# Performance work log

Hardware: AMD Instinct MI355X
Metric: run time of the kernel (lower is better)

Reference implementation:

```python
import jax, jax.numpy as jnp
import numpy as np

H = 8          # num_heads in nn.MultiheadAttention
TOP_K = 3
LN_EPS = 1e-5


def _layer_norm(x, gamma, beta):
    mu = x.mean(axis=-1, keepdims=True)
    var = ((x - mu) ** 2).mean(axis=-1, keepdims=True)
    return (x - mu) * jax.lax.rsqrt(var + LN_EPS) * gamma + beta


def setup_inputs() -> dict:
    key = jax.random.key(0)
    ks = jax.random.split(key, 12)
    B, T, D, N = 4, 4096, 1024, 64
    s = 0.02
    return {
        "current_frame": jax.random.normal(ks[0], (B, T, D), jnp.float32),
        "entity_memory": jax.random.normal(ks[1], (B, N, D), jnp.float32),
        "in_proj_w": jax.random.normal(ks[2], (3 * D, D), jnp.float32) * s,
        "in_proj_b": jax.random.normal(ks[3], (3 * D,), jnp.float32) * s,
        "out_proj_w": jax.random.normal(ks[4], (D, D), jnp.float32) * s,
        "out_proj_b": jax.random.normal(ks[5], (D,), jnp.float32) * s,
        "ln_gamma": jnp.ones((3, D), jnp.float32),
        "ln_beta": jnp.zeros((3, D), jnp.float32),
        "w1": jax.random.normal(ks[6], (3, 2 * D, D), jnp.float32) * s,
        "b1": jax.random.normal(ks[7], (3, 2 * D), jnp.float32) * s,
        "w2": jax.random.normal(ks[8], (3, D, 2 * D), jnp.float32) * s,
        "b2": jax.random.normal(ks[9], (3, D), jnp.float32) * s,
        "gate_w": jax.random.normal(ks[10], (D, 2 * D), jnp.float32) * s,
        "gate_b": jax.random.normal(ks[11], (D,), jnp.float32) * s,
    }


def reference(current_frame, entity_memory, in_proj_w, in_proj_b,
              out_proj_w, out_proj_b, ln_gamma, ln_beta, w1, b1, w2, b2,
              gate_w, gate_b):
    B, T, D = current_frame.shape
    N = entity_memory.shape[1]
    hd = D // H

    # --- nn.MultiheadAttention(q=frame, k=v=entity_memory), batch_first ---
    wq, wk, wv = in_proj_w[:D], in_proj_w[D:2 * D], in_proj_w[2 * D:]
    bq, bk, bv = in_proj_b[:D], in_proj_b[D:2 * D], in_proj_b[2 * D:]
    q = (current_frame @ wq.T + bq).reshape(B, T, H, hd).transpose(0, 2, 1, 3)
    k = (entity_memory @ wk.T + bk).reshape(B, N, H, hd).transpose(0, 2, 1, 3)
    v = (entity_memory @ wv.T + bv).reshape(B, N, H, hd).transpose(0, 2, 1, 3)
    scores = jnp.einsum('bhtd,bhnd->bhtn', q, k) / jnp.sqrt(jnp.float32(hd))
    attn = jax.nn.softmax(scores, axis=-1)                     # [B,H,T,N]
    ctx = jnp.einsum('bhtn,bhnd->bhtd', attn, v)
    ctx = ctx.transpose(0, 2, 1, 3).reshape(B, T, D)
    attended = ctx @ out_proj_w.T + out_proj_b
    attn_weights = attn.mean(axis=1)                           # avg over heads [B,T,N]

    # --- residual consistency MLP stack ---
    x = current_frame + attended
    for i in range(ln_gamma.shape[0]):
        h = _layer_norm(x, ln_gamma[i], ln_beta[i])
        h = jax.nn.gelu(h @ w1[i].T + b1[i], approximate=False)
        x = x + h @ w2[i].T + b2[i]

    # --- gated EMA entity-memory update ---
    frame_summary = current_frame.mean(axis=1, keepdims=True)   # [B,1,D]
    mem_summary = entity_memory.mean(axis=1, keepdims=True)     # [B,1,D]
    gate = jax.nn.sigmoid(
        jnp.concatenate([frame_summary, mem_summary], axis=-1) @ gate_w.T + gate_b)
    new_mem = gate * frame_summary + (1.0 - gate) * mem_summary  # [B,1,D]

    top_k = min(TOP_K, N)
    topk_idx = jax.lax.top_k(attn_weights.mean(axis=1), top_k)[1]  # [B,k]
    bidx = jnp.arange(B)[:, None]
    old = entity_memory[bidx, topk_idx]                          # [B,k,D]
    entity_memory = entity_memory.at[bidx, topk_idx].set(0.7 * old + 0.3 * new_mem)

    return x, entity_memory
```

## Files before the change

### kernel.cpp

```cpp
#include <hip/hip_runtime.h>
#include <hip/hip_bf16.h>
#include <cmath>

#define B_  4
#define T_  4096
#define D_  1024
#define N_  64
#define H_  8
#define HD_ 128
#define BT_ (B_*T_)
#define D2_ 2048

typedef __attribute__((ext_vector_type(8))) short bfrag8;
typedef __attribute__((ext_vector_type(4))) float f32x4;

__device__ __forceinline__ void gload_lds16(const void* g, void* l) {
    __builtin_amdgcn_global_load_lds(
        (const __attribute__((address_space(1))) unsigned int*)g,
        (__attribute__((address_space(3))) unsigned int*)l,
        16, 0, 0);
}

template<bool GELU, bool RES, bool OUTBF16>
__global__ __launch_bounds__(256) void gemm_bf16_kernel(
    const __hip_bfloat16* __restrict__ A, const __hip_bfloat16* __restrict__ Wt,
    const float* __restrict__ bias, const float* __restrict__ res,
    void* __restrict__ Cout, int M, int N, int K)
{
    __shared__ short As[128 * 32];
    __shared__ short Bs[128 * 32];

    const int tid = threadIdx.x;
    const int lane = tid & 63;
    const int wid = tid >> 6;
    const int wr = wid >> 1, wc = wid & 1;

    const int nwg = gridDim.x * gridDim.y;
    int lin = blockIdx.y * gridDim.x + blockIdx.x;
    lin = (lin & 7) * (nwg >> 3) + (lin >> 3);
    const int by = lin / gridDim.x;
    const int bx = lin - by * gridDim.x;
    const int m0 = by * 128;
    const int n0 = bx * 128;

    const int srow = tid >> 2;
    const int scol = (tid & 3) * 8;
    const short* Ag = (const short*)A;
    const short* Bg = (const short*)Wt;

    const int frow = lane & 15;
    const int fk   = (lane >> 4) * 8;

    f32x4 acc[4][4] = {};

    for (int k0 = 0; k0 < K; k0 += 32) {
        __syncthreads();
        gload_lds16(Ag + (size_t)(m0 + srow) * K + k0 + scol,       &As[tid * 8]);
        gload_lds16(Ag + (size_t)(m0 + 64 + srow) * K + k0 + scol,  &As[2048 + tid * 8]);
        gload_lds16(Bg + (size_t)(n0 + srow) * K + k0 + scol,       &Bs[tid * 8]);
        gload_lds16(Bg + (size_t)(n0 + 64 + srow) * K + k0 + scol,  &Bs[2048 + tid * 8]);
        __syncthreads();

        bfrag8 a[4], b[4];
#pragma unroll
        for (int i = 0; i < 4; ++i)
            a[i] = *(const bfrag8*)&As[(wr * 64 + i * 16 + frow) * 32 + fk];
#pragma unroll
        for (int j = 0; j < 4; ++j)
            b[j] = *(const bfrag8*)&Bs[(wc * 64 + j * 16 + frow) * 32 + fk];
#pragma unroll
        for (int i = 0; i < 4; ++i)
#pragma unroll
            for (int j = 0; j < 4; ++j)
                acc[i][j] = __builtin_amdgcn_mfma_f32_16x16x32_bf16(a[i], b[j], acc[i][j], 0, 0, 0);
    }

#pragma unroll
    for (int i = 0; i < 4; ++i) {
        const int rbase = m0 + wr * 64 + i * 16 + (lane >> 4) * 4;
#pragma unroll
        for (int r = 0; r < 4; ++r) {
            const size_t rowoff = (size_t)(rbase + r) * N;
#pragma unroll
            for (int j = 0; j < 4; ++j) {
                const int col = n0 + wc * 64 + j * 16 + (lane & 15);
                float v = acc[i][j][r] + bias[col];
                if (GELU) v = 0.5f * v * (1.0f + erff(v * 0.70710678118654752f));
                if (RES)  v += res[rowoff + col];
                if (OUTBF16) ((__hip_bfloat16*)Cout)[rowoff + col] = __float2bfloat16(v);
                else         ((float*)Cout)[rowoff + col] = v;
            }
        }
    }
}

__global__ __launch_bounds__(256) void cvt_kernel(
    const float* __restrict__ in, __hip_bfloat16* __restrict__ out, int n)
{
    const int i = (blockIdx.x * 256 + threadIdx.x) * 8;
    if (i >= n) return;
    const float4 v0 = *(const float4*)&in[i];
    const float4 v1 = *(const float4*)&in[i + 4];
    __hip_bfloat16 o[8];
    o[0] = __float2bfloat16(v0.x); o[1] = __float2bfloat16(v0.y);
    o[2] = __float2bfloat16(v0.z); o[3] = __float2bfloat16(v0.w);
    o[4] = __float2bfloat16(v1.x); o[5] = __float2bfloat16(v1.y);
    o[6] = __float2bfloat16(v1.z); o[7] = __float2bfloat16(v1.w);
    *(uint4*)&out[i] = *(uint4*)o;
}

__global__ __launch_bounds__(256) void ln_fused_kernel(
    const float* __restrict__ x, const float* __restrict__ g,
    const float* __restrict__ be, __hip_bfloat16* __restrict__ out)
{
    const int m = blockIdx.x;
    const int c = threadIdx.x * 4;
    const float4 v = *(const float4*)&x[(size_t)m * D_ + c];
    float s = v.x + v.y + v.z + v.w;
    float ss = v.x * v.x + v.y * v.y + v.z * v.z + v.w * v.w;
#pragma unroll
    for (int off = 32; off; off >>= 1) {
        s += __shfl_xor(s, off);
        ss += __shfl_xor(ss, off);
    }
    __shared__ float bs[4], bss[4];
    const int wave = threadIdx.x >> 6;
    if ((threadIdx.x & 63) == 0) { bs[wave] = s; bss[wave] = ss; }
    __syncthreads();
    const float S = bs[0] + bs[1] + bs[2] + bs[3];
    const float SS = bss[0] + bss[1] + bss[2] + bss[3];
    const float mean = S * (1.0f / D_);
    const float rstd = rsqrtf(SS * (1.0f / D_) - mean * mean + 1e-5f);
    const float4 gg = *(const float4*)&g[c];
    const float4 bb = *(const float4*)&be[c];
    __hip_bfloat16 o[4];
    o[0] = __float2bfloat16((v.x - mean) * rstd * gg.x + bb.x);
    o[1] = __float2bfloat16((v.y - mean) * rstd * gg.y + bb.y);
    o[2] = __float2bfloat16((v.z - mean) * rstd * gg.z + bb.z);
    o[3] = __float2bfloat16((v.w - mean) * rstd * gg.w + bb.w);
    *(uint2*)&out[(size_t)m * D_ + c] = *(uint2*)o;
}

__global__ __launch_bounds__(256) void vtrans_kernel(
    const __hip_bfloat16* __restrict__ vbb, __hip_bfloat16* __restrict__ vtb)
{
    const int bh = blockIdx.x;
    const int b = bh >> 3, h = bh & 7;
    for (int ii = threadIdx.x; ii < HD_ * N_; ii += 256) {
        const int d = ii >> 6, n = ii & 63;
        vtb[(size_t)bh * (HD_ * N_) + ii] =
            vbb[(size_t)(b * N_ + n) * D_ + h * HD_ + d];
    }
}

__global__ __launch_bounds__(256) void attn_mfma_kernel(
    const __hip_bfloat16* __restrict__ qb, const __hip_bfloat16* __restrict__ kbb,
    const __hip_bfloat16* __restrict__ vtb, __hip_bfloat16* __restrict__ ctxb,
    float* __restrict__ S)
{
    const int bh = blockIdx.y;
    const int b = bh >> 3, hh = bh & 7;
    const int t0 = blockIdx.x * 128;

    __shared__ short Ql[128 * 128];
    __shared__ short Kl[64 * 128];
    __shared__ short Vtl[128 * 64];
    __shared__ __hip_bfloat16 Pl[128 * 64];

    const int tid = threadIdx.x;
    const int lane = tid & 63;
    const int wid = tid >> 6;

    const short* qg = (const short*)qb;
    for (int s = wid; s < 32; s += 4) {
        const int row = 4 * s + (lane >> 4);
        const int col8 = (lane & 15) ^ (row & 7);
        gload_lds16(qg + ((size_t)(b * T_ + t0 + row)) * D_ + hh * HD_ + col8 * 8,
                    &Ql[s * 512 + lane * 8]);
    }
    const short* kg = (const short*)kbb;
    for (int s = wid; s < 16; s += 4) {
        const int row = 4 * s + (lane >> 4);
        const int col8 = (lane & 15) ^ (row & 7);
        gload_lds16(kg + ((size_t)(b * N_ + row)) * D_ + hh * HD_ + col8 * 8,
                    &Kl[s * 512 + lane * 8]);
    }
    const short* vg = (const short*)vtb + (size_t)bh * (HD_ * N_);
    for (int s = wid; s < 16; s += 4) {
        const int row = 8 * s + (lane >> 3);
        const int col8 = (lane & 7) ^ (row & 7);
        gload_lds16(vg + row * 64 + col8 * 8, &Vtl[s * 512 + lane * 8]);
    }
    __syncthreads();

    const int frow = lane & 15;
    const int fk8  = lane >> 4;

    f32x4 acc[2][4] = {};
#pragma unroll
    for (int ks = 0; ks < 4; ++ks) {
        bfrag8 a[2], bf[4];
#pragma unroll
        for (int i = 0; i < 2; ++i) {
            const int row = wid * 32 + i * 16 + frow;
            const int col8 = (ks * 4 + fk8) ^ (row & 7);
            a[i] = *(const bfrag8*)&Ql[row * 128 + col8 * 8];
        }
#pragma unroll
        for (int j = 0; j < 4; ++j) {
            const int row = j * 16 + frow;
            const int col8 = (ks * 4 + fk8) ^ (row & 7);
            bf[j] = *(const bfrag8*)&Kl[row * 128 + col8 * 8];
        }
#pragma unroll
        for (int i = 0; i < 2; ++i)
#pragma unroll
            for (int j = 0; j < 4; ++j)
                acc[i][j] = __builtin_amdgcn_mfma_f32_16x16x32_bf16(a[i], bf[j], acc[i][j], 0, 0, 0);
    }

    const float scale = 0.088388347648318441f;
    float accS[4] = {0.f, 0.f, 0.f, 0.f};
#pragma unroll
    for (int i = 0; i < 2; ++i) {
#pragma unroll
        for (int r = 0; r < 4; ++r) {
            float sv[4];
            float m = -INFINITY;
#pragma unroll
            for (int j = 0; j < 4; ++j) { sv[j] = acc[i][j][r] * scale; m = fmaxf(m, sv[j]); }
#pragma unroll
            for (int off = 1; off < 16; off <<= 1) m = fmaxf(m, __shfl_xor(m, off));
            float sum = 0.f;
#pragma unroll
            for (int j = 0; j < 4; ++j) { sv[j] = __expf(sv[j] - m); sum += sv[j]; }
#pragma unroll
            for (int off = 1; off < 16; off <<= 1) sum += __shfl_xor(sum, off);
            const float inv = 1.0f / sum;
            const int row = wid * 32 + i * 16 + (lane >> 4) * 4 + r;
#pragma unroll
            for (int j = 0; j < 4; ++j) {
                const float pn = sv[j] * inv;
                accS[j] += pn;
                const int col = j * 16 + (lane & 15);
                Pl[row * 64 + (((col >> 3) ^ (row & 7)) << 3) + (col & 7)] = __float2bfloat16(pn);
            }
        }
    }
#pragma unroll
    for (int j = 0; j < 4; ++j) {
        float v = accS[j];
        v += __shfl_xor(v, 16);
        v += __shfl_xor(v, 32);
        if (lane < 16)
            atomicAdd(&S[b * N_ + j * 16 + lane], v * (1.0f / (H_ * (float)T_)));
    }
    __syncthreads();

    f32x4 acc2[2][8] = {};
#pragma unroll
    for (int ks = 0; ks < 2; ++ks) {
        bfrag8 pa[2];
#pragma unroll
        for (int i = 0; i < 2; ++i) {
            const int row = wid * 32 + i * 16 + frow;
            const int col8 = (ks * 4 + fk8) ^ (row & 7);
            pa[i] = *(const bfrag8*)&Pl[row * 64 + col8 * 8];
        }
#pragma unroll
        for (int j = 0; j < 8; ++j) {
            const int row = j * 16 + frow;
            const int col8 = (ks * 4 + fk8) ^ (row & 7);
            const bfrag8 vv = *(const bfrag8*)&Vtl[row * 64 + col8 * 8];
#pragma unroll
            for (int i = 0; i < 2; ++i)
                acc2[i][j] = __builtin_amdgcn_mfma_f32_16x16x32_bf16(pa[i], vv, acc2[i][j], 0, 0, 0);
        }
    }

    short* Cl = Ql;
#pragma unroll
    for (int i = 0; i < 2; ++i)
#pragma unroll
        for (int r = 0; r < 4; ++r) {
            const int row = wid * 32 + i * 16 + (lane >> 4) * 4 + r;
#pragma unroll
            for (int j = 0; j < 8; ++j) {
                __hip_bfloat16 hv = __float2bfloat16(acc2[i][j][r]);
                Cl[row * 128 + j * 16 + (lane & 15)] = *(short*)&hv;
            }
        }
    __syncthreads();
    short* cg = (short*)ctxb;
#pragma unroll
    for (int s = 0; s < 8; ++s) {
        const int c = s * 256 + tid;
        const int row = c >> 4;
        const int slot = c & 15;
        *(uint4*)&cg[((size_t)(b * T_ + t0 + row)) * D_ + hh * HD_ + slot * 8] =
            *(const uint4*)&Cl[row * 128 + slot * 8];
    }
}

__global__ __launch_bounds__(256) void frame_summary_kernel(
    const float* __restrict__ cf, float* __restrict__ fs)
{
    const int b = blockIdx.x;
    const int d = blockIdx.y * 256 + threadIdx.x;
    const int t0 = blockIdx.z * 512;
    float s = 0.0f;
    for (int t = t0; t < t0 + 512; ++t)
        s += cf[((size_t)(b * T_ + t)) * D_ + d];
    atomicAdd(&fs[b * D_ + d], s * (1.0f / (float)T_));
}

__global__ __launch_bounds__(256) void mem_summary_kernel(
    const float* __restrict__ em, float* __restrict__ ms)
{
    const int b = blockIdx.x;
    const int d = blockIdx.y * 256 + threadIdx.x;
    float s = 0.0f;
#pragma unroll 4
    for (int n = 0; n < N_; ++n)
        s += em[((size_t)(b * N_ + n)) * D_ + d];
    ms[b * D_ + d] = s * (1.0f / (float)N_);
}

__global__ __launch_bounds__(256) void gate_kernel(
    const float* __restrict__ fs, const float* __restrict__ ms,
    const float* __restrict__ gw, const float* __restrict__ gb,
    float* __restrict__ nm)
{
    const int b = blockIdx.x;
    const int d = blockIdx.y * 256 + threadIdx.x;
    const float* wrow = gw + (size_t)d * D2_;
    const float* f = fs + b * D_;
    const float* mm = ms + b * D_;
    float g = gb[d];
    for (int j = 0; j < D_; ++j) g += f[j] * wrow[j];
    for (int j = 0; j < D_; ++j) g += mm[j] * wrow[D_ + j];
    const float sig = 1.0f / (1.0f + __expf(-g));
    nm[b * D_ + d] = sig * f[d] + (1.0f - sig) * mm[d];
}

__global__ __launch_bounds__(256) void topk_update_kernel(
    const float* __restrict__ S, const float* __restrict__ em,
    const float* __restrict__ nm, float* __restrict__ emo)
{
    const int b = blockIdx.x;
    __shared__ int topi[3];
    const int tid = threadIdx.x;
    if (tid < 64) {
        float sv = S[b * N_ + tid];
#pragma unroll
        for (int k = 0; k < 3; ++k) {
            float v = sv;
            int idx = tid;
#pragma unroll
            for (int off = 32; off; off >>= 1) {
                const float ov = __shfl_xor(v, off);
                const int oi = __shfl_xor(idx, off);
                if (ov > v || (ov == v && oi < idx)) { v = ov; idx = oi; }
            }
            if (tid == 0) topi[k] = idx;
            if (tid == idx) sv = -INFINITY;
        }
    }
    __syncthreads();
    const int i0 = topi[0], i1 = topi[1], i2 = topi[2];
    const float4* emb = (const float4*)(em + (size_t)b * N_ * D_);
    const float4* nmb = (const float4*)(nm + (size_t)b * D_);
    float4* outb = (float4*)(emo + (size_t)b * N_ * D_);
    for (int idx = tid; idx < N_ * D_ / 4; idx += 256) {
        const int n = idx >> 8;
        const int d4 = idx & 255;
        float4 v = emb[idx];
        if (n == i0 || n == i1 || n == i2) {
            const float4 nv = nmb[d4];
            v.x = 0.7f * v.x + 0.3f * nv.x;
            v.y = 0.7f * v.y + 0.3f * nv.y;
            v.z = 0.7f * v.z + 0.3f * nv.z;
            v.w = 0.7f * v.w + 0.3f * nv.w;
        }
        outb[idx] = v;
    }
}

extern "C" void kernel_launch(void* const* d_in, const int* in_sizes, int n_in,
                              void* d_out, int out_size, void* d_ws, size_t ws_size,
                              hipStream_t stream)
{
    const float* cf  = (const float*)d_in[0];
    const float* em  = (const float*)d_in[1];
    const float* ipw = (const float*)d_in[2];
    const float* ipb = (const float*)d_in[3];
    const float* opw = (const float*)d_in[4];
    const float* opb = (const float*)d_in[5];
    const float* lng = (const float*)d_in[6];
    const float* lnb = (const float*)d_in[7];
    const float* w1  = (const float*)d_in[8];
    const float* b1  = (const float*)d_in[9];
    const float* w2  = (const float*)d_in[10];
    const float* b2  = (const float*)d_in[11];
    const float* gw  = (const float*)d_in[12];
    const float* gb  = (const float*)d_in[13];

    float* x   = (float*)d_out;
    float* emo = x + (size_t)BT_ * D_;

    char* w = (char*)d_ws;
    __hip_bfloat16* h    = (__hip_bfloat16*)w;
    __hip_bfloat16* qbuf = (__hip_bfloat16*)w;
    w += 67108864;
    __hip_bfloat16* actb = (__hip_bfloat16*)w; w += 33554432;
    __hip_bfloat16* ipwb = (__hip_bfloat16*)w; w += 6291456;
    __hip_bfloat16* opwb = (__hip_bfloat16*)w; w += 2097152;
    __hip_bfloat16* w1b  = (__hip_bfloat16*)w; w += 12582912;
    __hip_bfloat16* w2b  = (__hip_bfloat16*)w; w += 12582912;
    __hip_bfloat16* emb  = (__hip_bfloat16*)w; w += 524288;
    __hip_bfloat16* kbb  = (__hip_bfloat16*)w; w += 524288;
    __hip_bfloat16* vbb  = (__hip_bfloat16*)w; w += 524288;
    __hip_bfloat16* vtb  = (__hip_bfloat16*)w; w += 524288;
    float* S  = (float*)w; w += 1024;
    float* fs = (float*)w; w += 16384;
    float* ms = (float*)w; w += 16384;
    float* nm = (float*)w; w += 16384;

    hipMemsetAsync(S, 0, (256 + 4096) * sizeof(float), stream);

    const dim3 blk(256);

    cvt_kernel<<<8192, blk, 0, stream>>>(cf, actb, BT_ * D_);
    cvt_kernel<<<128,  blk, 0, stream>>>(em, emb, B_ * N_ * D_);
    cvt_kernel<<<1536, blk, 0, stream>>>(ipw, ipwb, 3 * D_ * D_);
    cvt_kernel<<<512,  blk, 0, stream>>>(opw, opwb, D_ * D_);
    cvt_kernel<<<3072, blk, 0, stream>>>(w1, w1b, 3 * D2_ * D_);
    cvt_kernel<<<3072, blk, 0, stream>>>(w2, w2b, 3 * D_ * D2_);

    gemm_bf16_kernel<false, false, true><<<dim3(8, 128), blk, 0, stream>>>(
        actb, ipwb, ipb, nullptr, qbuf, BT_, D_, D_);
    gemm_bf16_kernel<false, false, true><<<dim3(8, 2), blk, 0, stream>>>(
        emb, ipwb + D_ * D_, ipb + D_, nullptr, kbb, B_ * N_, D_, D_);
    gemm_bf16_kernel<false, false, true><<<dim3(8, 2), blk, 0, stream>>>(
        emb, ipwb + 2 * D_ * D_, ipb + 2 * D_, nullptr, vbb, B_ * N_, D_, D_);
    vtrans_kernel<<<B_ * H_, blk, 0, stream>>>(vbb, vtb);

    attn_mfma_kernel<<<dim3(T_ / 128, B_ * H_), blk, 0, stream>>>(
        qbuf, kbb, vtb, actb, S);

    gemm_bf16_kernel<false, true, false><<<dim3(8, 128), blk, 0, stream>>>(
        actb, opwb, opb, cf, x, BT_, D_, D_);

    for (int i = 0; i < 3; ++i) {
        ln_fused_kernel<<<BT_, blk, 0, stream>>>(
            x, lng + i * D_, lnb + i * D_, actb);
        gemm_bf16_kernel<true, false, true><<<dim3(16, 128), blk, 0, stream>>>(
            actb, w1b + (size_t)i * D2_ * D_, b1 + i * D2_, nullptr, h,
            BT_, D2_, D_);
        gemm_bf16_kernel<false, true, false><<<dim3(8, 128), blk, 0, stream>>>(
            h, w2b + (size_t)i * D_ * D2_, b2 + i * D_, x, x,
            BT_, D_, D2_);
    }

    frame_summary_kernel<<<dim3(B_, 4, 8), blk, 0, stream>>>(cf, fs);
    mem_summary_kernel<<<dim3(B_, 4), blk, 0, stream>>>(em, ms);
    gate_kernel<<<dim3(B_, 4), blk, 0, stream>>>(fs, ms, gw, gb, nm);
    topk_update_kernel<<<B_, blk, 0, stream>>>(S, em, nm, emo);
}
```

Baseline: 1.282 ms.

## Enlarge GEMM tiles to 256x256 with double-buffered swizzled LDS staging

The bf16 GEMM moves from 128x128 tiles with K-step 32 and 256 threads to 256x256 tiles with K-step 64 and 512 threads. The global-to-LDS loads are double-buffered so the next K tile is fetched while MFMAs run on the current one, and an XOR swizzle on the LDS column offset is meant to avoid bank conflicts. Bias loads are hoisted out of the epilogue loop. Each thread now holds 128 accumulator floats and each block uses 128KB of LDS, so occupancy drops to one block per CU. The launch bound asks for two blocks per CU, which may force register spills.

```diff
diff --git a/kernel.cpp b/kernel.cpp
--- a/kernel.cpp
+++ b/kernel.cpp
@@ -22,69 +22,96 @@
 }
 
 template<bool GELU, bool RES, bool OUTBF16>
-__global__ __launch_bounds__(256) void gemm_bf16_kernel(
+__global__ __launch_bounds__(512, 2) void gemm_bf16_kernel(
     const __hip_bfloat16* __restrict__ A, const __hip_bfloat16* __restrict__ Wt,
     const float* __restrict__ bias, const float* __restrict__ res,
     void* __restrict__ Cout, int M, int N, int K)
 {
-    __shared__ short As[128 * 32];
-    __shared__ short Bs[128 * 32];
+    __shared__ short As[2 * 256 * 64];
+    __shared__ short Bs[2 * 256 * 64];
 
     const int tid = threadIdx.x;
     const int lane = tid & 63;
     const int wid = tid >> 6;
-    const int wr = wid >> 1, wc = wid & 1;
+    const int wr = wid >> 2;
+    const int wc = wid & 3;
 
     const int nwg = gridDim.x * gridDim.y;
     int lin = blockIdx.y * gridDim.x + blockIdx.x;
-    lin = (lin & 7) * (nwg >> 3) + (lin >> 3);
+    if ((nwg & 7) == 0) lin = (lin & 7) * (nwg >> 3) + (lin >> 3);
     const int by = lin / gridDim.x;
     const int bx = lin - by * gridDim.x;
-    const int m0 = by * 128;
-    const int n0 = bx * 128;
-
-    const int srow = tid >> 2;
-    const int scol = (tid & 3) * 8;
+    const int m0 = by * 256;
+    const int n0 = bx * 256;
+
     const short* Ag = (const short*)A;
     const short* Bg = (const short*)Wt;
 
     const int frow = lane & 15;
-    const int fk   = (lane >> 4) * 8;
-
-    f32x4 acc[4][4] = {};
-
-    for (int k0 = 0; k0 < K; k0 += 32) {
+    const int fk8  = lane >> 4;
+
+    f32x4 acc[8][4] = {};
+
+    const int nt = K >> 6;
+
+    auto STAGE = [&](int t) {
+        const int kb = t << 6;
+        short* Ab = &As[(t & 1) * 16384];
+        short* Bb = &Bs[(t & 1) * 16384];
+#pragma unroll
+        for (int s = 0; s < 4; ++s) {
+            const int L = s * 512 + tid;
+            const int row = L >> 3, p = L & 7;
+            const int g8 = ((p ^ (row & 7)) << 3);
+            gload_lds16(Ag + (size_t)(m0 + row) * K + kb + g8, &Ab[L * 8]);
+            gload_lds16(Bg + (size_t)(n0 + row) * K + kb + g8, &Bb[L * 8]);
+        }
+    };
+
+    STAGE(0);
+    asm volatile("s_waitcnt vmcnt(0)" ::: "memory");
+    __syncthreads();
+
+    for (int t = 0; t < nt; ++t) {
+        if (t + 1 < nt) STAGE(t + 1);
+        const short* Ab = &As[(t & 1) * 16384];
+        const short* Bb = &Bs[(t & 1) * 16384];
+        for (int kk = 0; kk < 2; ++kk) {
+            bfrag8 a[8], b[4];
+#pragma unroll
+            for (int i = 0; i < 8; ++i) {
+                const int row = wr * 128 + i * 16 + frow;
+                a[i] = *(const bfrag8*)&Ab[row * 64 + (((kk * 4 + fk8) ^ (row & 7)) << 3)];
+            }
+#pragma unroll
+            for (int j = 0; j < 4; ++j) {
+                const int row = wc * 64 + j * 16 + frow;
+                b[j] = *(const bfrag8*)&Bb[row * 64 + (((kk * 4 + fk8) ^ (row & 7)) << 3)];
+            }
+#pragma unroll
+            for (int i = 0; i < 8; ++i)
+#pragma unroll
+                for (int j = 0; j < 4; ++j)
+                    acc[i][j] = __builtin_amdgcn_mfma_f32_16x16x32_bf16(a[i], b[j], acc[i][j], 0, 0, 0);
+        }
+        asm volatile("s_waitcnt vmcnt(0)" ::: "memory");
         __syncthreads();
-        gload_lds16(Ag + (size_t)(m0 + srow) * K + k0 + scol,       &As[tid * 8]);
-        gload_lds16(Ag + (size_t)(m0 + 64 + srow) * K + k0 + scol,  &As[2048 + tid * 8]);
-        gload_lds16(Bg + (size_t)(n0 + srow) * K + k0 + scol,       &Bs[tid * 8]);
-        gload_lds16(Bg + (size_t)(n0 + 64 + srow) * K + k0 + scol,  &Bs[2048 + tid * 8]);
-        __syncthreads();
-
-        bfrag8 a[4], b[4];
-#pragma unroll
-        for (int i = 0; i < 4; ++i)
-            a[i] = *(const bfrag8*)&As[(wr * 64 + i * 16 + frow) * 32 + fk];
-#pragma unroll
-        for (int j = 0; j < 4; ++j)
-            b[j] = *(const bfrag8*)&Bs[(wc * 64 + j * 16 + frow) * 32 + fk];
-#pragma unroll
-        for (int i = 0; i < 4; ++i)
-#pragma unroll
-            for (int j = 0; j < 4; ++j)
-                acc[i][j] = __builtin_amdgcn_mfma_f32_16x16x32_bf16(a[i], b[j], acc[i][j], 0, 0, 0);
-    }
-
-#pragma unroll
-    for (int i = 0; i < 4; ++i) {
-        const int rbase = m0 + wr * 64 + i * 16 + (lane >> 4) * 4;
+    }
+
+    float bias4[4];
+#pragma unroll
+    for (int j = 0; j < 4; ++j)
+        bias4[j] = bias[n0 + wc * 64 + j * 16 + (lane & 15)];
+#pragma unroll
+    for (int i = 0; i < 8; ++i) {
+        const int rbase = m0 + wr * 128 + i * 16 + (lane >> 4) * 4;
 #pragma unroll
         for (int r = 0; r < 4; ++r) {
             const size_t rowoff = (size_t)(rbase + r) * N;
 #pragma unroll
             for (int j = 0; j < 4; ++j) {
                 const int col = n0 + wc * 64 + j * 16 + (lane & 15);
-                float v = acc[i][j][r] + bias[col];
+                float v = acc[i][j][r] + bias4[j];
                 if (GELU) v = 0.5f * v * (1.0f + erff(v * 0.70710678118654752f));
                 if (RES)  v += res[rowoff + col];
                 if (OUTBF16) ((__hip_bfloat16*)Cout)[rowoff + col] = __float2bfloat16(v);
@@ -429,6 +456,7 @@
     hipMemsetAsync(S, 0, (256 + 4096) * sizeof(float), stream);
 
     const dim3 blk(256);
+    const dim3 blk512(512);
 
     cvt_kernel<<<8192, blk, 0, stream>>>(cf, actb, BT_ * D_);
     cvt_kernel<<<128,  blk, 0, stream>>>(em, emb, B_ * N_ * D_);
@@ -437,27 +465,27 @@
     cvt_kernel<<<3072, blk, 0, stream>>>(w1, w1b, 3 * D2_ * D_);
     cvt_kernel<<<3072, blk, 0, stream>>>(w2, w2b, 3 * D_ * D2_);
 
-    gemm_bf16_kernel<false, false, true><<<dim3(8, 128), blk, 0, stream>>>(
+    gemm_bf16_kernel<false, false, true><<<dim3(4, 64), blk512, 0, stream>>>(
         actb, ipwb, ipb, nullptr, qbuf, BT_, D_, D_);
-    gemm_bf16_kernel<false, false, true><<<dim3(8, 2), blk, 0, stream>>>(
+    gemm_bf16_kernel<false, false, true><<<dim3(4, 1), blk512, 0, stream>>>(
         emb, ipwb + D_ * D_, ipb + D_, nullptr, kbb, B_ * N_, D_, D_);
-    gemm_bf16_kernel<false, false, true><<<dim3(8, 2), blk, 0, stream>>>(
+    gemm_bf16_kernel<false, false, true><<<dim3(4, 1), blk512, 0, stream>>>(
         emb, ipwb + 2 * D_ * D_, ipb + 2 * D_, nullptr, vbb, B_ * N_, D_, D_);
     vtrans_kernel<<<B_ * H_, blk, 0, stream>>>(vbb, vtb);
 
     attn_mfma_kernel<<<dim3(T_ / 128, B_ * H_), blk, 0, stream>>>(
         qbuf, kbb, vtb, actb, S);
 
-    gemm_bf16_kernel<false, true, false><<<dim3(8, 128), blk, 0, stream>>>(
+    gemm_bf16_kernel<false, true, false><<<dim3(4, 64), blk512, 0, stream>>>(
         actb, opwb, opb, cf, x, BT_, D_, D_);
 
     for (int i = 0; i < 3; ++i) {
         ln_fused_kernel<<<BT_, blk, 0, stream>>>(
             x, lng + i * D_, lnb + i * D_, actb);
-        gemm_bf16_kernel<true, false, true><<<dim3(16, 128), blk, 0, stream>>>(
+        gemm_bf16_kernel<true, false, true><<<dim3(8, 64), blk512, 0, stream>>>(
             actb, w1b + (size_t)i * D2_ * D_, b1 + i * D2_, nullptr, h,
             BT_, D2_, D_);
-        gemm_bf16_kernel<false, true, false><<<dim3(8, 128), blk, 0, stream>>>(
+        gemm_bf16_kernel<false, true, false><<<dim3(4, 64), blk512, 0, stream>>>(
             h, w2b + (size_t)i * D_ * D2_, b2 + i * D_, x, x,
             BT_, D_, D2_);
     }
```

Measured after the change: 1.166 ms. -9.0%, faster.

## Double GEMM K-tile to 64 with XOR-swizzled LDS and fuse K/V projections

Applied to the files above, without the earlier changes.

The bf16 GEMM now stages 64-wide K slices per iteration instead of 32, using an XOR swizzle on the LDS layout to avoid bank conflicts. This halves the number of barrier pairs per K loop and gives two MFMA sub-steps per load phase. The K and V projection GEMMs are merged into one launch writing a combined KV buffer, and the attention and transpose kernels index into it. The grid remap is now guarded for grid sizes that are not multiples of 8. LDS use per block doubles, which may reduce occupancy.

```diff
diff --git a/kernel.cpp b/kernel.cpp
--- a/kernel.cpp
+++ b/kernel.cpp
@@ -27,8 +27,8 @@
     const float* __restrict__ bias, const float* __restrict__ res,
     void* __restrict__ Cout, int M, int N, int K)
 {
-    __shared__ short As[128 * 32];
-    __shared__ short Bs[128 * 32];
+    __shared__ short As[128 * 64];
+    __shared__ short Bs[128 * 64];
 
     const int tid = threadIdx.x;
     const int lane = tid & 63;
@@ -37,42 +37,55 @@
 
     const int nwg = gridDim.x * gridDim.y;
     int lin = blockIdx.y * gridDim.x + blockIdx.x;
-    lin = (lin & 7) * (nwg >> 3) + (lin >> 3);
+    if ((nwg & 7) == 0) lin = (lin & 7) * (nwg >> 3) + (lin >> 3);
     const int by = lin / gridDim.x;
     const int bx = lin - by * gridDim.x;
     const int m0 = by * 128;
     const int n0 = bx * 128;
 
-    const int srow = tid >> 2;
-    const int scol = (tid & 3) * 8;
-    const short* Ag = (const short*)A;
-    const short* Bg = (const short*)Wt;
+    const short* Ag = (const short*)A + (size_t)m0 * K;
+    const short* Bg = (const short*)Wt + (size_t)n0 * K;
 
     const int frow = lane & 15;
-    const int fk   = (lane >> 4) * 8;
+    const int fk8  = lane >> 4;
 
     f32x4 acc[4][4] = {};
 
-    for (int k0 = 0; k0 < K; k0 += 32) {
+    for (int kb = 0; kb < K; kb += 64) {
         __syncthreads();
-        gload_lds16(Ag + (size_t)(m0 + srow) * K + k0 + scol,       &As[tid * 8]);
-        gload_lds16(Ag + (size_t)(m0 + 64 + srow) * K + k0 + scol,  &As[2048 + tid * 8]);
-        gload_lds16(Bg + (size_t)(n0 + srow) * K + k0 + scol,       &Bs[tid * 8]);
-        gload_lds16(Bg + (size_t)(n0 + 64 + srow) * K + k0 + scol,  &Bs[2048 + tid * 8]);
+#pragma unroll
+        for (int s = 0; s < 4; ++s) {
+            const int L = s * 256 + tid;
+            const int row = L >> 3, p = L & 7;
+            gload_lds16(Ag + (size_t)row * K + kb + ((p ^ (row & 7)) << 3), &As[L * 8]);
+        }
+#pragma unroll
+        for (int s = 0; s < 4; ++s) {
+            const int L = s * 256 + tid;
+            const int row = L >> 3, p = L & 7;
+            gload_lds16(Bg + (size_t)row * K + kb + ((p ^ (row & 7)) << 3), &Bs[L * 8]);
+        }
         __syncthreads();
 
-        bfrag8 a[4], b[4];
-#pragma unroll
-        for (int i = 0; i < 4; ++i)
-            a[i] = *(const bfrag8*)&As[(wr * 64 + i * 16 + frow) * 32 + fk];
-#pragma unroll
-        for (int j = 0; j < 4; ++j)
-            b[j] = *(const bfrag8*)&Bs[(wc * 64 + j * 16 + frow) * 32 + fk];
-#pragma unroll
-        for (int i = 0; i < 4; ++i)
-#pragma unroll
-            for (int j = 0; j < 4; ++j)
-                acc[i][j] = __builtin_amdgcn_mfma_f32_16x16x32_bf16(a[i], b[j], acc[i][j], 0, 0, 0);
+#pragma unroll
+        for (int kk = 0; kk < 2; ++kk) {
+            bfrag8 a[4], b[4];
+#pragma unroll
+            for (int i = 0; i < 4; ++i) {
+                const int row = wr * 64 + i * 16 + frow;
+                a[i] = *(const bfrag8*)&As[row * 64 + (((kk * 4 + fk8) ^ (row & 7)) << 3)];
+            }
+#pragma unroll
+            for (int j = 0; j < 4; ++j) {
+                const int row = wc * 64 + j * 16 + frow;
+                b[j] = *(const bfrag8*)&Bs[row * 64 + (((kk * 4 + fk8) ^ (row & 7)) << 3)];
+            }
+#pragma unroll
+            for (int i = 0; i < 4; ++i)
+#pragma unroll
+                for (int j = 0; j < 4; ++j)
+                    acc[i][j] = __builtin_amdgcn_mfma_f32_16x16x32_bf16(a[i], b[j], acc[i][j], 0, 0, 0);
+        }
     }
 
 #pragma unroll
@@ -142,19 +155,19 @@
 }
 
 __global__ __launch_bounds__(256) void vtrans_kernel(
-    const __hip_bfloat16* __restrict__ vbb, __hip_bfloat16* __restrict__ vtb)
+    const __hip_bfloat16* __restrict__ kv, __hip_bfloat16* __restrict__ vtb)
 {
     const int bh = blockIdx.x;
     const int b = bh >> 3, h = bh & 7;
     for (int ii = threadIdx.x; ii < HD_ * N_; ii += 256) {
         const int d = ii >> 6, n = ii & 63;
         vtb[(size_t)bh * (HD_ * N_) + ii] =
-            vbb[(size_t)(b * N_ + n) * D_ + h * HD_ + d];
+            kv[(size_t)(b * N_ + n) * D2_ + 1024 + h * HD_ + d];
     }
 }
 
 __global__ __launch_bounds__(256) void attn_mfma_kernel(
-    const __hip_bfloat16* __restrict__ qb, const __hip_bfloat16* __restrict__ kbb,
+    const __hip_bfloat16* __restrict__ qb, const __hip_bfloat16* __restrict__ kv,
     const __hip_bfloat16* __restrict__ vtb, __hip_bfloat16* __restrict__ ctxb,
     float* __restrict__ S)
 {
@@ -178,11 +191,11 @@
         gload_lds16(qg + ((size_t)(b * T_ + t0 + row)) * D_ + hh * HD_ + col8 * 8,
                     &Ql[s * 512 + lane * 8]);
     }
-    const short* kg = (const short*)kbb;
+    const short* kg = (const short*)kv;
     for (int s = wid; s < 16; s += 4) {
         const int row = 4 * s + (lane >> 4);
         const int col8 = (lane & 15) ^ (row & 7);
-        gload_lds16(kg + ((size_t)(b * N_ + row)) * D_ + hh * HD_ + col8 * 8,
+        gload_lds16(kg + ((size_t)(b * N_ + row)) * D2_ + hh * HD_ + col8 * 8,
                     &Kl[s * 512 + lane * 8]);
     }
     const short* vg = (const short*)vtb + (size_t)bh * (HD_ * N_);
@@ -418,8 +431,7 @@
     __hip_bfloat16* w1b  = (__hip_bfloat16*)w; w += 12582912;
     __hip_bfloat16* w2b  = (__hip_bfloat16*)w; w += 12582912;
     __hip_bfloat16* emb  = (__hip_bfloat16*)w; w += 524288;
-    __hip_bfloat16* kbb  = (__hip_bfloat16*)w; w += 524288;
-    __hip_bfloat16* vbb  = (__hip_bfloat16*)w; w += 524288;
+    __hip_bfloat16* kvb  = (__hip_bfloat16*)w; w += 1048576;
     __hip_bfloat16* vtb  = (__hip_bfloat16*)w; w += 524288;
     float* S  = (float*)w; w += 1024;
     float* fs = (float*)w; w += 16384;
@@ -439,14 +451,12 @@
 
     gemm_bf16_kernel<false, false, true><<<dim3(8, 128), blk, 0, stream>>>(
         actb, ipwb, ipb, nullptr, qbuf, BT_, D_, D_);
-    gemm_bf16_kernel<false, false, true><<<dim3(8, 2), blk, 0, stream>>>(
-        emb, ipwb + D_ * D_, ipb + D_, nullptr, kbb, B_ * N_, D_, D_);
-    gemm_bf16_kernel<false, false, true><<<dim3(8, 2), blk, 0, stream>>>(
-        emb, ipwb + 2 * D_ * D_, ipb + 2 * D_, nullptr, vbb, B_ * N_, D_, D_);
-    vtrans_kernel<<<B_ * H_, blk, 0, stream>>>(vbb, vtb);
+    gemm_bf16_kernel<false, false, true><<<dim3(16, 2), blk, 0, stream>>>(
+        emb, ipwb + D_ * D_, ipb + D_, nullptr, kvb, B_ * N_, D2_, D_);
+    vtrans_kernel<<<B_ * H_, blk, 0, stream>>>(kvb, vtb);
 
     attn_mfma_kernel<<<dim3(T_ / 128, B_ * H_), blk, 0, stream>>>(
-        qbuf, kbb, vtb, actb, S);
+        qbuf, kvb, vtb, actb, S);
 
     gemm_bf16_kernel<false, true, false><<<dim3(8, 128), blk, 0, stream>>>(
         actb, opwb, opb, cf, x, BT_, D_, D_);
```

New measurement: 1.124 ms. 1.14x faster.
